# Kernel optimization log

Measured on AMD Instinct MI355X. Metric: run time of the kernel, lower is better.

Reference implementation:

```python
import jax, jax.numpy as jnp
from jax import lax
import numpy as np

# kz = (7, 3): kh is a 1x7 horizontal kernel, kv is a 3x1 vertical kernel
KH = (1, 7)
KV = (3, 1)


def _morph(x, ksz, op, init):
    # F.unfold zero-pads, so padded border values participate in the min/max
    ph, pw = ksz[0] // 2, ksz[1] // 2
    xp = jnp.pad(x, ((0, 0), (0, 0), (ph, ph), (pw, pw)))
    return lax.reduce_window(xp, init, op, (1, 1, ksz[0], ksz[1]), (1, 1, 1, 1), 'VALID')


def _erode(x, ksz):
    return _morph(x, ksz, lax.min, np.float32(np.inf))


def _dilate(x, ksz):
    return _morph(x, ksz, lax.max, np.float32(-np.inf))


def _calphi(x):
    dil = _dilate(x, KH)                                   # horizontal dilation (1x7)
    thr = dil.mean(axis=(2, 3), keepdims=True)             # per-image mean of dilation
    bi = ((x > thr) & (x == dil)).astype(x.dtype)          # horizontal local-max binarization
    return _dilate(_erode(bi, KV), KV)                     # morphological opening with 3x1


def setup_inputs() -> dict:
    key = jax.random.key(0)
    x = jax.random.normal(key, (8, 1, 2048, 2048), dtype=jnp.float32)
    return {"x": x}


def reference(x):
    s1 = _calphi(x).sum()
    s2 = _calphi(jnp.swapaxes(x, 2, 3)).sum()
    return s1 < s2
```

## Files before the change

### kernel.cpp

```cpp
#include <hip/hip_runtime.h>
#include <cstdint>

#define NEG_INF (-__builtin_inff())

static constexpr int H = 2048;
static constexpr int W = 2048;
static constexpr int STR = 248;
static constexpr int RC  = 8;
static constexpr int NR  = RC + 6;

struct F4 { float x, y, z, w; };

__device__ __forceinline__ F4 ld4(const float* __restrict__ p) {
    float4 v = *reinterpret_cast<const float4*>(p);
    return {v.x, v.y, v.z, v.w};
}

__device__ __forceinline__ float fmax3(float a, float b, float c) {
    return fmaxf(fmaxf(a, b), c);
}

__device__ __forceinline__ void hmax7_4(float a0, float a1, float a2,
                                        float a3, float a4, float a5, float a6,
                                        float a7, float a8, float a9,
                                        float& m0, float& m1, float& m2, float& m3) {
    float p23 = fmaxf(a2, a3), p45 = fmaxf(a4, a5), p67 = fmaxf(a6, a7);
    float q25 = fmaxf(p23, p45), q47 = fmaxf(p45, p67);
    m0 = fmax3(fmaxf(a0, a1), q25, a6);
    m1 = fmax3(fmaxf(a1, a2), fmax3(a3, a4, a5), fmaxf(a6, a7));
    m2 = fmax3(p23, q47, a8);
    m3 = fmax3(fmaxf(a3, a4), fmax3(a5, a6, a7), fmaxf(a8, a9));
}

struct Setup {
    int c4, cA, cmask, imask;
    float pad0, pad1, pad2, pad3;
};

__device__ __forceinline__ Setup make_setup(int sIdx, int lane) {
    Setup s;
    const int cstart = sIdx * STR;
    s.c4 = cstart - 4 + lane * 4;
    s.cA = min(max(s.c4, 0), W - 4);
    s.cmask = 0; s.imask = 0;
#pragma unroll
    for (int k = 0; k < 4; ++k) {
        const int col = s.c4 + k;
        if (col >= cstart && col < cstart + STR && col < W) s.cmask |= 1 << k;
        if (col >= 0 && col < W)                            s.imask |= 1 << k;
    }
    s.pad0 = ((s.c4 + 0) < 3 || (s.c4 + 0) > W - 4) ? 0.f : NEG_INF;
    s.pad1 = ((s.c4 + 1) < 3 || (s.c4 + 1) > W - 4) ? 0.f : NEG_INF;
    s.pad2 = ((s.c4 + 2) < 3 || (s.c4 + 2) > W - 4) ? 0.f : NEG_INF;
    s.pad3 = ((s.c4 + 3) < 3 || (s.c4 + 3) > W - 4) ? 0.f : NEG_INF;
    return s;
}

__device__ __forceinline__ void load_rows(const float* __restrict__ img,
                                          int r0, const Setup& s, F4 (&cur)[NR]) {
#pragma unroll
    for (int t = 0; t < NR; ++t) {
        const int irc = min(max(r0 - 3 + t, 0), H - 1);
        cur[t] = ld4(img + (size_t)irc * W + s.cA);
    }
#pragma unroll
    for (int t = 0; t < NR; ++t)
        asm volatile("" : "+v"(cur[t].x), "+v"(cur[t].y), "+v"(cur[t].z), "+v"(cur[t].w));
    if (s.imask != 0xF) {
#pragma unroll
        for (int t = 0; t < NR; ++t) {
            if (!(s.imask & 1)) cur[t].x = NEG_INF;
            if (!(s.imask & 2)) cur[t].y = NEG_INF;
            if (!(s.imask & 4)) cur[t].z = NEG_INF;
            if (!(s.imask & 8)) cur[t].w = NEG_INF;
        }
    }
#pragma unroll
    for (int t = 0; t < NR; ++t) {
        if (t < 3 || t >= NR - 3) {
            const int ir = r0 - 3 + t;
            if (ir < 0 || ir >= H) cur[t] = {NEG_INF, NEG_INF, NEG_INF, NEG_INF};
        }
    }
}

__global__ __launch_bounds__(256) void k_sums(const float* __restrict__ x,
                                              double* __restrict__ sums) {
    const int tid = threadIdx.x, lane = tid & 63, wid = tid >> 6;
    const int sIdx = blockIdx.x;
    const int rr   = blockIdx.y * 4 + wid;
    const int b    = blockIdx.z;
    const int r0   = rr * RC;
    const float* img = x + (size_t)b * H * W;
    const Setup s = make_setup(sIdx, lane);

    F4 cur[NR];
    load_rows(img, r0, s, cur);

    float shf = 0.f, svf = 0.f;
#pragma unroll
    for (int t = 3; t < 3 + RC; ++t) {
        F4 c = cur[t];
        float la1 = __shfl_up(c.y, 1), la2 = __shfl_up(c.z, 1), la3 = __shfl_up(c.w, 1);
        float ra0 = __shfl_down(c.x, 1), ra1 = __shfl_down(c.y, 1), ra2 = __shfl_down(c.z, 1);
        float m0, m1, m2, m3;
        hmax7_4(la1, la2, la3, c.x, c.y, c.z, c.w, ra0, ra1, ra2, m0, m1, m2, m3);
        m0 = fmaxf(m0, s.pad0); m1 = fmaxf(m1, s.pad1);
        m2 = fmaxf(m2, s.pad2); m3 = fmaxf(m3, s.pad3);
        shf += ((s.cmask & 1) ? m0 : 0.f) + ((s.cmask & 2) ? m1 : 0.f)
             + ((s.cmask & 4) ? m2 : 0.f) + ((s.cmask & 8) ? m3 : 0.f);
    }
#pragma unroll
    for (int jj = 0; jj < RC; ++jj) {
        const int j = r0 + jj;
        const float rpad = (j < 3 || j > H - 4) ? 0.f : NEG_INF;
        float mx = fmax3(fmax3(cur[jj].x, cur[jj+1].x, cur[jj+2].x),
                         fmax3(cur[jj+3].x, cur[jj+4].x, cur[jj+5].x), cur[jj+6].x);
        float my = fmax3(fmax3(cur[jj].y, cur[jj+1].y, cur[jj+2].y),
                         fmax3(cur[jj+3].y, cur[jj+4].y, cur[jj+5].y), cur[jj+6].y);
        float mz = fmax3(fmax3(cur[jj].z, cur[jj+1].z, cur[jj+2].z),
                         fmax3(cur[jj+3].z, cur[jj+4].z, cur[jj+5].z), cur[jj+6].z);
        float mw = fmax3(fmax3(cur[jj].w, cur[jj+1].w, cur[jj+2].w),
                         fmax3(cur[jj+3].w, cur[jj+4].w, cur[jj+5].w), cur[jj+6].w);
        mx = fmaxf(mx, rpad); my = fmaxf(my, rpad);
        mz = fmaxf(mz, rpad); mw = fmaxf(mw, rpad);
        svf += ((s.cmask & 1) ? mx : 0.f) + ((s.cmask & 2) ? my : 0.f)
             + ((s.cmask & 4) ? mz : 0.f) + ((s.cmask & 8) ? mw : 0.f);
    }

    double sh = (double)shf, sv = (double)svf;
    for (int off = 32; off > 0; off >>= 1) {
        sh += __shfl_down(sh, off);
        sv += __shfl_down(sv, off);
    }
    if (lane == 0) {
        const int bk = rr & 63;
        atomicAdd(&sums[(b)      * 64 + bk], sh);
        atomicAdd(&sums[(8 + b)  * 64 + bk], sv);
    }
}

__global__ void k_thr(const double* __restrict__ sums, float* __restrict__ thr) {
    const int p = threadIdx.x;
    if (p < 16) {
        const double* s = sums + p * 64;
        double a = 0.0;
        for (int i = 0; i < 64; ++i) a += s[i];
        thr[p] = (float)(a * (1.0 / ((double)H * (double)W)));
    }
}

__global__ __launch_bounds__(256) void k_counts(const float* __restrict__ x,
                                                const float* __restrict__ thr,
                                                unsigned int* __restrict__ cnts) {
    const int tid = threadIdx.x, lane = tid & 63, wid = tid >> 6;
    const int sIdx = blockIdx.x;
    const int rr   = blockIdx.y * 4 + wid;
    const int b    = blockIdx.z;
    const int r0   = rr * RC;
    const float* img = x + (size_t)b * H * W;
    const Setup s = make_setup(sIdx, lane);
    const float thr1 = thr[b], thr2 = thr[8 + b];

    F4 cur[NR];
    load_rows(img, r0, s, cur);

    unsigned bc0 = 0, bc1 = 0, bc2 = 0, bc3 = 0;
#pragma unroll
    for (int t = 1; t < NR - 1; ++t) {
        F4 c = cur[t];
        float la1 = __shfl_up(c.y, 1), la2 = __shfl_up(c.z, 1), la3 = __shfl_up(c.w, 1);
        float ra0 = __shfl_down(c.x, 1), ra1 = __shfl_down(c.y, 1), ra2 = __shfl_down(c.z, 1);
        float m0, m1, m2, m3;
        hmax7_4(la1, la2, la3, c.x, c.y, c.z, c.w, ra0, ra1, ra2, m0, m1, m2, m3);
        m0 = fmaxf(m0, s.pad0); m1 = fmaxf(m1, s.pad1);
        m2 = fmaxf(m2, s.pad2); m3 = fmaxf(m3, s.pad3);
        bc0 |= (c.x > thr1 && c.x == m0) ? (1u << t) : 0u;
        bc1 |= (c.y > thr1 && c.y == m1) ? (1u << t) : 0u;
        bc2 |= (c.z > thr1 && c.z == m2) ? (1u << t) : 0u;
        bc3 |= (c.w > thr1 && c.w == m3) ? (1u << t) : 0u;
    }
    const unsigned rowm = ((1u << RC) - 1u) << 3;
    unsigned e0 = bc0 & (bc0 << 1) & (bc0 >> 1);
    unsigned e1 = bc1 & (bc1 << 1) & (bc1 >> 1);
    unsigned e2 = bc2 & (bc2 << 1) & (bc2 >> 1);
    unsigned e3 = bc3 & (bc3 << 1) & (bc3 >> 1);
    unsigned o0 = e0 | (e0 << 1) | (e0 >> 1);
    unsigned o1_ = e1 | (e1 << 1) | (e1 >> 1);
    unsigned o2_ = e2 | (e2 << 1) | (e2 >> 1);
    unsigned o3_ = e3 | (e3 << 1) | (e3 >> 1);
    unsigned cnt1 = ((s.cmask & 1) ? __popc(o0  & rowm) : 0u)
                  + ((s.cmask & 2) ? __popc(o1_ & rowm) : 0u)
                  + ((s.cmask & 4) ? __popc(o2_ & rowm) : 0u)
                  + ((s.cmask & 8) ? __popc(o3_ & rowm) : 0u);

    unsigned d0 = 0, d1 = 0, d2 = 0, d3 = 0;
#pragma unroll
    for (int jj = 0; jj < RC; ++jj) {
        const int j = r0 + jj;
        const float rpad = (j < 3 || j > H - 4) ? 0.f : NEG_INF;
        float mx = fmax3(fmax3(cur[jj].x, cur[jj+1].x, cur[jj+2].x),
                         fmax3(cur[jj+3].x, cur[jj+4].x, cur[jj+5].x), cur[jj+6].x);
        float my = fmax3(fmax3(cur[jj].y, cur[jj+1].y, cur[jj+2].y),
                         fmax3(cur[jj+3].y, cur[jj+4].y, cur[jj+5].y), cur[jj+6].y);
        float mz = fmax3(fmax3(cur[jj].z, cur[jj+1].z, cur[jj+2].z),
                         fmax3(cur[jj+3].z, cur[jj+4].z, cur[jj+5].z), cur[jj+6].z);
        float mw = fmax3(fmax3(cur[jj].w, cur[jj+1].w, cur[jj+2].w),
                         fmax3(cur[jj+3].w, cur[jj+4].w, cur[jj+5].w), cur[jj+6].w);
        mx = fmaxf(mx, rpad); my = fmaxf(my, rpad);
        mz = fmaxf(mz, rpad); mw = fmaxf(mw, rpad);
        F4 ce = cur[jj + 3];
        d0 |= (ce.x > thr2 && ce.x == mx) ? (1u << jj) : 0u;
        d1 |= (ce.y > thr2 && ce.y == my) ? (1u << jj) : 0u;
        d2 |= (ce.z > thr2 && ce.z == mz) ? (1u << jj) : 0u;
        d3 |= (ce.w > thr2 && ce.w == mw) ? (1u << jj) : 0u;
    }
    const unsigned pz = __shfl_up(d2, 1), pw = __shfl_up(d3, 1);
    const unsigned n0 = __shfl_down(d0, 1), n1 = __shfl_down(d1, 1);
    const unsigned em1 = pz & pw & d0;
    const unsigned f0  = pw & d0 & d1;
    const unsigned f1  = d0 & d1 & d2;
    const unsigned f2  = d1 & d2 & d3;
    const unsigned f3  = d2 & d3 & n0;
    const unsigned fp4 = d3 & n0 & n1;
    const unsigned q0 = em1 | f0 | f1;
    const unsigned q1 = f0 | f1 | f2;
    const unsigned q2 = f1 | f2 | f3;
    const unsigned q3 = f2 | f3 | fp4;
    unsigned cnt2 = ((s.cmask & 1) ? __popc(q0) : 0u)
                  + ((s.cmask & 2) ? __popc(q1) : 0u)
                  + ((s.cmask & 4) ? __popc(q2) : 0u)
                  + ((s.cmask & 8) ? __popc(q3) : 0u);

    for (int off = 32; off > 0; off >>= 1) {
        cnt1 += __shfl_down(cnt1, off);
        cnt2 += __shfl_down(cnt2, off);
    }
    if (lane == 0) {
        const int bkt = (rr * 9 + sIdx) & 127;
        atomicAdd(&cnts[bkt],       cnt1);
        atomicAdd(&cnts[128 + bkt], cnt2);
    }
}

__global__ void k_final(const unsigned int* __restrict__ cnts,
                        int* __restrict__ out) {
    const int l = threadIdx.x;
    unsigned a = cnts[l] + cnts[64 + l];
    unsigned c = cnts[128 + l] + cnts[192 + l];
    for (int off = 32; off > 0; off >>= 1) {
        a += __shfl_down(a, off);
        c += __shfl_down(c, off);
    }
    if (l == 0) out[0] = (a < c) ? 1 : 0;
}

extern "C" void kernel_launch(void* const* d_in, const int* in_sizes, int n_in,
                              void* d_out, int out_size, void* d_ws, size_t ws_size,
                              hipStream_t stream) {
    const float* x = (const float*)d_in[0];
    int* out = (int*)d_out;
    double* sums = (double*)d_ws;
    float* thr = (float*)((char*)d_ws + 8192);
    unsigned int* cnts = (unsigned int*)((char*)d_ws + 8448);

    hipMemsetAsync(d_ws, 0, 16384, stream);

    k_sums  <<<dim3(9, 64, 8), 256, 0, stream>>>(x, sums);
    k_thr   <<<1, 16, 0, stream>>>(sums, thr);
    k_counts<<<dim3(9, 64, 8), 256, 0, stream>>>(x, thr, cnts);
    k_final <<<1, 64, 0, stream>>>(cnts, out);
}
```

Measured before the change: 247.1 us.

## Double rows per wave and replace atomics with per-block partial sums

Raises rows per wave from 8 to 16, which halves the grid and cuts the share of redundant halo-row loads (6 extra rows per chunk). Each block now reduces its four waves' results in shared memory and writes one slot per block, replacing global atomics into buckets and removing the workspace memset. The threshold and final kernels are rewritten to reduce over the per-block slots. The trade-offs are more registers per thread (22 float4 rows held) and fewer blocks to fill the GPU.

```diff
diff --git a/kernel.cpp b/kernel.cpp
--- a/kernel.cpp
+++ b/kernel.cpp
@@ -6,8 +6,11 @@
 static constexpr int H = 2048;
 static constexpr int W = 2048;
 static constexpr int STR = 248;
-static constexpr int RC  = 8;
+static constexpr int RC  = 16;
 static constexpr int NR  = RC + 6;
+static constexpr int NCH = H / RC;
+static constexpr int GY  = NCH / 4;
+static constexpr int NBLK = 9 * GY * 8;
 
 struct F4 { float x, y, z, w; };
 
@@ -82,6 +85,10 @@
             if (ir < 0 || ir >= H) cur[t] = {NEG_INF, NEG_INF, NEG_INF, NEG_INF};
         }
     }
+}
+
+__device__ __forceinline__ int blk_id() {
+    return (blockIdx.z * GY + blockIdx.y) * 9 + blockIdx.x;
 }
 
 __global__ __launch_bounds__(256) void k_sums(const float* __restrict__ x,
@@ -133,21 +140,28 @@
         sh += __shfl_down(sh, off);
         sv += __shfl_down(sv, off);
     }
-    if (lane == 0) {
-        const int bk = rr & 63;
-        atomicAdd(&sums[(b)      * 64 + bk], sh);
-        atomicAdd(&sums[(8 + b)  * 64 + bk], sv);
+    __shared__ double sdh[4], sdv[4];
+    if (lane == 0) { sdh[wid] = sh; sdv[wid] = sv; }
+    __syncthreads();
+    if (tid == 0) {
+        const int blk = blk_id();
+        sums[blk]        = sdh[0] + sdh[1] + sdh[2] + sdh[3];
+        sums[NBLK + blk] = sdv[0] + sdv[1] + sdv[2] + sdv[3];
     }
 }
 
 __global__ void k_thr(const double* __restrict__ sums, float* __restrict__ thr) {
-    const int p = threadIdx.x;
-    if (p < 16) {
-        const double* s = sums + p * 64;
-        double a = 0.0;
-        for (int i = 0; i < 64; ++i) a += s[i];
-        thr[p] = (float)(a * (1.0 / ((double)H * (double)W)));
-    }
+    const int tid = threadIdx.x;
+    const int pair = tid >> 4, l16 = tid & 15;
+    const double* base = sums + (pair < 8 ? pair * 288 : NBLK + (pair - 8) * 288);
+    double a = 0.0;
+#pragma unroll
+    for (int k = 0; k < 18; ++k) a += base[l16 + k * 16];
+    a += __shfl_down(a, 8);
+    a += __shfl_down(a, 4);
+    a += __shfl_down(a, 2);
+    a += __shfl_down(a, 1);
+    if (l16 == 0) thr[pair] = (float)(a * (1.0 / ((double)H * (double)W)));
 }
 
 __global__ __launch_bounds__(256) void k_counts(const float* __restrict__ x,
@@ -236,23 +250,37 @@
         cnt1 += __shfl_down(cnt1, off);
         cnt2 += __shfl_down(cnt2, off);
     }
-    if (lane == 0) {
-        const int bkt = (rr * 9 + sIdx) & 127;
-        atomicAdd(&cnts[bkt],       cnt1);
-        atomicAdd(&cnts[128 + bkt], cnt2);
+    __shared__ unsigned sc1[4], sc2[4];
+    if (lane == 0) { sc1[wid] = cnt1; sc2[wid] = cnt2; }
+    __syncthreads();
+    if (tid == 0) {
+        const int blk = blk_id();
+        cnts[blk]        = sc1[0] + sc1[1] + sc1[2] + sc1[3];
+        cnts[NBLK + blk] = sc2[0] + sc2[1] + sc2[2] + sc2[3];
     }
 }
 
 __global__ void k_final(const unsigned int* __restrict__ cnts,
                         int* __restrict__ out) {
-    const int l = threadIdx.x;
-    unsigned a = cnts[l] + cnts[64 + l];
-    unsigned c = cnts[128 + l] + cnts[192 + l];
+    const int tid = threadIdx.x;
+    unsigned a = 0, c = 0;
+    for (int i = tid; i < NBLK; i += 256) {
+        a += cnts[i];
+        c += cnts[NBLK + i];
+    }
     for (int off = 32; off > 0; off >>= 1) {
         a += __shfl_down(a, off);
         c += __shfl_down(c, off);
     }
-    if (l == 0) out[0] = (a < c) ? 1 : 0;
+    __shared__ unsigned sa[4], sc[4];
+    const int lane = tid & 63, wid = tid >> 6;
+    if (lane == 0) { sa[wid] = a; sc[wid] = c; }
+    __syncthreads();
+    if (tid == 0) {
+        unsigned A = sa[0] + sa[1] + sa[2] + sa[3];
+        unsigned C = sc[0] + sc[1] + sc[2] + sc[3];
+        out[0] = (A < C) ? 1 : 0;
+    }
 }
 
 extern "C" void kernel_launch(void* const* d_in, const int* in_sizes, int n_in,
@@ -261,13 +289,11 @@
     const float* x = (const float*)d_in[0];
     int* out = (int*)d_out;
     double* sums = (double*)d_ws;
-    float* thr = (float*)((char*)d_ws + 8192);
-    unsigned int* cnts = (unsigned int*)((char*)d_ws + 8448);
-
-    hipMemsetAsync(d_ws, 0, 16384, stream);
-
-    k_sums  <<<dim3(9, 64, 8), 256, 0, stream>>>(x, sums);
-    k_thr   <<<1, 16, 0, stream>>>(sums, thr);
-    k_counts<<<dim3(9, 64, 8), 256, 0, stream>>>(x, thr, cnts);
-    k_final <<<1, 64, 0, stream>>>(cnts, out);
-}
+    float* thr = (float*)((char*)d_ws + 2 * NBLK * 8);
+    unsigned int* cnts = (unsigned int*)((char*)d_ws + 2 * NBLK * 8 + 256);
+
+    k_sums  <<<dim3(9, GY, 8), 256, 0, stream>>>(x, sums);
+    k_thr   <<<1, 256, 0, stream>>>(sums, thr);
+    k_counts<<<dim3(9, GY, 8), 256, 0, stream>>>(x, thr, cnts);
+    k_final <<<1, 256, 0, stream>>>(cnts, out);
+}
```

New measurement: 265.3 us. 1.07x slower.

## Fuse four kernels into one cooperative persistent kernel with grid syncs

Applied to the files above, without the earlier changes.

Replaces the separate sums, threshold, counts and final kernels with one cooperative persistent kernel. Blocks loop over tasks and use grid-wide syncs between phases, and each block computes the thresholds itself into shared memory. This removes three kernel launch gaps and the tiny serial threshold and final kernels. The cost is two grid barriers and __launch_bounds__(256,4) register pressure, which may limit occupancy.

```diff
diff --git a/kernel.cpp b/kernel.cpp
--- a/kernel.cpp
+++ b/kernel.cpp
@@ -1,5 +1,8 @@
 #include <hip/hip_runtime.h>
+#include <hip/hip_cooperative_groups.h>
 #include <cstdint>
+
+namespace cg = cooperative_groups;
 
 #define NEG_INF (-__builtin_inff())
 
@@ -8,6 +11,8 @@
 static constexpr int STR = 248;
 static constexpr int RC  = 8;
 static constexpr int NR  = RC + 6;
+static constexpr int NCH = H / RC;
+static constexpr int NTASK = 9 * (NCH / 4) * 8;
 
 struct F4 { float x, y, z, w; };
 
@@ -84,175 +89,188 @@
     }
 }
 
-__global__ __launch_bounds__(256) void k_sums(const float* __restrict__ x,
-                                              double* __restrict__ sums) {
+__device__ __forceinline__ void task_decode(int beta, int& b, int& rrG, int& sIdx) {
+    b = beta / 576;
+    const int rem = beta % 576;
+    rrG = rem / 9;
+    sIdx = rem % 9;
+}
+
+__global__ __launch_bounds__(256, 4)
+void k_fused(const float* __restrict__ x, double* __restrict__ sums,
+             unsigned int* __restrict__ cnts, int* __restrict__ out) {
+    cg::grid_group grid = cg::this_grid();
     const int tid = threadIdx.x, lane = tid & 63, wid = tid >> 6;
-    const int sIdx = blockIdx.x;
-    const int rr   = blockIdx.y * 4 + wid;
-    const int b    = blockIdx.z;
-    const int r0   = rr * RC;
-    const float* img = x + (size_t)b * H * W;
-    const Setup s = make_setup(sIdx, lane);
-
-    F4 cur[NR];
-    load_rows(img, r0, s, cur);
-
-    float shf = 0.f, svf = 0.f;
-#pragma unroll
-    for (int t = 3; t < 3 + RC; ++t) {
-        F4 c = cur[t];
-        float la1 = __shfl_up(c.y, 1), la2 = __shfl_up(c.z, 1), la3 = __shfl_up(c.w, 1);
-        float ra0 = __shfl_down(c.x, 1), ra1 = __shfl_down(c.y, 1), ra2 = __shfl_down(c.z, 1);
-        float m0, m1, m2, m3;
-        hmax7_4(la1, la2, la3, c.x, c.y, c.z, c.w, ra0, ra1, ra2, m0, m1, m2, m3);
-        m0 = fmaxf(m0, s.pad0); m1 = fmaxf(m1, s.pad1);
-        m2 = fmaxf(m2, s.pad2); m3 = fmaxf(m3, s.pad3);
-        shf += ((s.cmask & 1) ? m0 : 0.f) + ((s.cmask & 2) ? m1 : 0.f)
-             + ((s.cmask & 4) ? m2 : 0.f) + ((s.cmask & 8) ? m3 : 0.f);
-    }
-#pragma unroll
-    for (int jj = 0; jj < RC; ++jj) {
-        const int j = r0 + jj;
-        const float rpad = (j < 3 || j > H - 4) ? 0.f : NEG_INF;
-        float mx = fmax3(fmax3(cur[jj].x, cur[jj+1].x, cur[jj+2].x),
-                         fmax3(cur[jj+3].x, cur[jj+4].x, cur[jj+5].x), cur[jj+6].x);
-        float my = fmax3(fmax3(cur[jj].y, cur[jj+1].y, cur[jj+2].y),
-                         fmax3(cur[jj+3].y, cur[jj+4].y, cur[jj+5].y), cur[jj+6].y);
-        float mz = fmax3(fmax3(cur[jj].z, cur[jj+1].z, cur[jj+2].z),
-                         fmax3(cur[jj+3].z, cur[jj+4].z, cur[jj+5].z), cur[jj+6].z);
-        float mw = fmax3(fmax3(cur[jj].w, cur[jj+1].w, cur[jj+2].w),
-                         fmax3(cur[jj+3].w, cur[jj+4].w, cur[jj+5].w), cur[jj+6].w);
-        mx = fmaxf(mx, rpad); my = fmaxf(my, rpad);
-        mz = fmaxf(mz, rpad); mw = fmaxf(mw, rpad);
-        svf += ((s.cmask & 1) ? mx : 0.f) + ((s.cmask & 2) ? my : 0.f)
-             + ((s.cmask & 4) ? mz : 0.f) + ((s.cmask & 8) ? mw : 0.f);
-    }
-
-    double sh = (double)shf, sv = (double)svf;
-    for (int off = 32; off > 0; off >>= 1) {
-        sh += __shfl_down(sh, off);
-        sv += __shfl_down(sv, off);
-    }
-    if (lane == 0) {
-        const int bk = rr & 63;
-        atomicAdd(&sums[(b)      * 64 + bk], sh);
-        atomicAdd(&sums[(8 + b)  * 64 + bk], sv);
-    }
-}
-
-__global__ void k_thr(const double* __restrict__ sums, float* __restrict__ thr) {
-    const int p = threadIdx.x;
-    if (p < 16) {
-        const double* s = sums + p * 64;
-        double a = 0.0;
-        for (int i = 0; i < 64; ++i) a += s[i];
-        thr[p] = (float)(a * (1.0 / ((double)H * (double)W)));
-    }
-}
-
-__global__ __launch_bounds__(256) void k_counts(const float* __restrict__ x,
-                                                const float* __restrict__ thr,
-                                                unsigned int* __restrict__ cnts) {
-    const int tid = threadIdx.x, lane = tid & 63, wid = tid >> 6;
-    const int sIdx = blockIdx.x;
-    const int rr   = blockIdx.y * 4 + wid;
-    const int b    = blockIdx.z;
-    const int r0   = rr * RC;
-    const float* img = x + (size_t)b * H * W;
-    const Setup s = make_setup(sIdx, lane);
-    const float thr1 = thr[b], thr2 = thr[8 + b];
-
-    F4 cur[NR];
-    load_rows(img, r0, s, cur);
-
-    unsigned bc0 = 0, bc1 = 0, bc2 = 0, bc3 = 0;
-#pragma unroll
-    for (int t = 1; t < NR - 1; ++t) {
-        F4 c = cur[t];
-        float la1 = __shfl_up(c.y, 1), la2 = __shfl_up(c.z, 1), la3 = __shfl_up(c.w, 1);
-        float ra0 = __shfl_down(c.x, 1), ra1 = __shfl_down(c.y, 1), ra2 = __shfl_down(c.z, 1);
-        float m0, m1, m2, m3;
-        hmax7_4(la1, la2, la3, c.x, c.y, c.z, c.w, ra0, ra1, ra2, m0, m1, m2, m3);
-        m0 = fmaxf(m0, s.pad0); m1 = fmaxf(m1, s.pad1);
-        m2 = fmaxf(m2, s.pad2); m3 = fmaxf(m3, s.pad3);
-        bc0 |= (c.x > thr1 && c.x == m0) ? (1u << t) : 0u;
-        bc1 |= (c.y > thr1 && c.y == m1) ? (1u << t) : 0u;
-        bc2 |= (c.z > thr1 && c.z == m2) ? (1u << t) : 0u;
-        bc3 |= (c.w > thr1 && c.w == m3) ? (1u << t) : 0u;
-    }
-    const unsigned rowm = ((1u << RC) - 1u) << 3;
-    unsigned e0 = bc0 & (bc0 << 1) & (bc0 >> 1);
-    unsigned e1 = bc1 & (bc1 << 1) & (bc1 >> 1);
-    unsigned e2 = bc2 & (bc2 << 1) & (bc2 >> 1);
-    unsigned e3 = bc3 & (bc3 << 1) & (bc3 >> 1);
-    unsigned o0 = e0 | (e0 << 1) | (e0 >> 1);
-    unsigned o1_ = e1 | (e1 << 1) | (e1 >> 1);
-    unsigned o2_ = e2 | (e2 << 1) | (e2 >> 1);
-    unsigned o3_ = e3 | (e3 << 1) | (e3 >> 1);
-    unsigned cnt1 = ((s.cmask & 1) ? __popc(o0  & rowm) : 0u)
-                  + ((s.cmask & 2) ? __popc(o1_ & rowm) : 0u)
-                  + ((s.cmask & 4) ? __popc(o2_ & rowm) : 0u)
-                  + ((s.cmask & 8) ? __popc(o3_ & rowm) : 0u);
-
-    unsigned d0 = 0, d1 = 0, d2 = 0, d3 = 0;
-#pragma unroll
-    for (int jj = 0; jj < RC; ++jj) {
-        const int j = r0 + jj;
-        const float rpad = (j < 3 || j > H - 4) ? 0.f : NEG_INF;
-        float mx = fmax3(fmax3(cur[jj].x, cur[jj+1].x, cur[jj+2].x),
-                         fmax3(cur[jj+3].x, cur[jj+4].x, cur[jj+5].x), cur[jj+6].x);
-        float my = fmax3(fmax3(cur[jj].y, cur[jj+1].y, cur[jj+2].y),
-                         fmax3(cur[jj+3].y, cur[jj+4].y, cur[jj+5].y), cur[jj+6].y);
-        float mz = fmax3(fmax3(cur[jj].z, cur[jj+1].z, cur[jj+2].z),
-                         fmax3(cur[jj+3].z, cur[jj+4].z, cur[jj+5].z), cur[jj+6].z);
-        float mw = fmax3(fmax3(cur[jj].w, cur[jj+1].w, cur[jj+2].w),
-                         fmax3(cur[jj+3].w, cur[jj+4].w, cur[jj+5].w), cur[jj+6].w);
-        mx = fmaxf(mx, rpad); my = fmaxf(my, rpad);
-        mz = fmaxf(mz, rpad); mw = fmaxf(mw, rpad);
-        F4 ce = cur[jj + 3];
-        d0 |= (ce.x > thr2 && ce.x == mx) ? (1u << jj) : 0u;
-        d1 |= (ce.y > thr2 && ce.y == my) ? (1u << jj) : 0u;
-        d2 |= (ce.z > thr2 && ce.z == mz) ? (1u << jj) : 0u;
-        d3 |= (ce.w > thr2 && ce.w == mw) ? (1u << jj) : 0u;
-    }
-    const unsigned pz = __shfl_up(d2, 1), pw = __shfl_up(d3, 1);
-    const unsigned n0 = __shfl_down(d0, 1), n1 = __shfl_down(d1, 1);
-    const unsigned em1 = pz & pw & d0;
-    const unsigned f0  = pw & d0 & d1;
-    const unsigned f1  = d0 & d1 & d2;
-    const unsigned f2  = d1 & d2 & d3;
-    const unsigned f3  = d2 & d3 & n0;
-    const unsigned fp4 = d3 & n0 & n1;
-    const unsigned q0 = em1 | f0 | f1;
-    const unsigned q1 = f0 | f1 | f2;
-    const unsigned q2 = f1 | f2 | f3;
-    const unsigned q3 = f2 | f3 | fp4;
-    unsigned cnt2 = ((s.cmask & 1) ? __popc(q0) : 0u)
-                  + ((s.cmask & 2) ? __popc(q1) : 0u)
-                  + ((s.cmask & 4) ? __popc(q2) : 0u)
-                  + ((s.cmask & 8) ? __popc(q3) : 0u);
-
-    for (int off = 32; off > 0; off >>= 1) {
-        cnt1 += __shfl_down(cnt1, off);
-        cnt2 += __shfl_down(cnt2, off);
-    }
-    if (lane == 0) {
-        const int bkt = (rr * 9 + sIdx) & 127;
-        atomicAdd(&cnts[bkt],       cnt1);
-        atomicAdd(&cnts[128 + bkt], cnt2);
-    }
-}
-
-__global__ void k_final(const unsigned int* __restrict__ cnts,
-                        int* __restrict__ out) {
-    const int l = threadIdx.x;
-    unsigned a = cnts[l] + cnts[64 + l];
-    unsigned c = cnts[128 + l] + cnts[192 + l];
-    for (int off = 32; off > 0; off >>= 1) {
-        a += __shfl_down(a, off);
-        c += __shfl_down(c, off);
-    }
-    if (l == 0) out[0] = (a < c) ? 1 : 0;
+    __shared__ float thrS[16];
+
+    for (int beta = blockIdx.x; beta < NTASK; beta += gridDim.x) {
+        int b, rrG, sIdx;
+        task_decode(beta, b, rrG, sIdx);
+        const int rr = rrG * 4 + wid, r0 = rr * RC;
+        const float* img = x + (size_t)b * H * W;
+        const Setup s = make_setup(sIdx, lane);
+
+        F4 cur[NR];
+        load_rows(img, r0, s, cur);
+
+        float shf = 0.f, svf = 0.f;
+#pragma unroll
+        for (int t = 3; t < 3 + RC; ++t) {
+            F4 c = cur[t];
+            float la1 = __shfl_up(c.y, 1), la2 = __shfl_up(c.z, 1), la3 = __shfl_up(c.w, 1);
+            float ra0 = __shfl_down(c.x, 1), ra1 = __shfl_down(c.y, 1), ra2 = __shfl_down(c.z, 1);
+            float m0, m1, m2, m3;
+            hmax7_4(la1, la2, la3, c.x, c.y, c.z, c.w, ra0, ra1, ra2, m0, m1, m2, m3);
+            m0 = fmaxf(m0, s.pad0); m1 = fmaxf(m1, s.pad1);
+            m2 = fmaxf(m2, s.pad2); m3 = fmaxf(m3, s.pad3);
+            shf += ((s.cmask & 1) ? m0 : 0.f) + ((s.cmask & 2) ? m1 : 0.f)
+                 + ((s.cmask & 4) ? m2 : 0.f) + ((s.cmask & 8) ? m3 : 0.f);
+        }
+#pragma unroll
+        for (int jj = 0; jj < RC; ++jj) {
+            const int j = r0 + jj;
+            const float rpad = (j < 3 || j > H - 4) ? 0.f : NEG_INF;
+            float mx = fmax3(fmax3(cur[jj].x, cur[jj+1].x, cur[jj+2].x),
+                             fmax3(cur[jj+3].x, cur[jj+4].x, cur[jj+5].x), cur[jj+6].x);
+            float my = fmax3(fmax3(cur[jj].y, cur[jj+1].y, cur[jj+2].y),
+                             fmax3(cur[jj+3].y, cur[jj+4].y, cur[jj+5].y), cur[jj+6].y);
+            float mz = fmax3(fmax3(cur[jj].z, cur[jj+1].z, cur[jj+2].z),
+                             fmax3(cur[jj+3].z, cur[jj+4].z, cur[jj+5].z), cur[jj+6].z);
+            float mw = fmax3(fmax3(cur[jj].w, cur[jj+1].w, cur[jj+2].w),
+                             fmax3(cur[jj+3].w, cur[jj+4].w, cur[jj+5].w), cur[jj+6].w);
+            mx = fmaxf(mx, rpad); my = fmaxf(my, rpad);
+            mz = fmaxf(mz, rpad); mw = fmaxf(mw, rpad);
+            svf += ((s.cmask & 1) ? mx : 0.f) + ((s.cmask & 2) ? my : 0.f)
+                 + ((s.cmask & 4) ? mz : 0.f) + ((s.cmask & 8) ? mw : 0.f);
+        }
+
+        double sh = (double)shf, sv = (double)svf;
+        for (int off = 32; off > 0; off >>= 1) {
+            sh += __shfl_down(sh, off);
+            sv += __shfl_down(sv, off);
+        }
+        if (lane == 0) {
+            const int bkt = (rr * 9 + sIdx) & 63;
+            atomicAdd(&sums[(b)     * 64 + bkt], sh);
+            atomicAdd(&sums[(8 + b) * 64 + bkt], sv);
+        }
+    }
+
+    __threadfence();
+    grid.sync();
+
+    {
+        const int pair = tid >> 4, l16 = tid & 15;
+        double a = sums[pair * 64 + l16]      + sums[pair * 64 + l16 + 16]
+                 + sums[pair * 64 + l16 + 32] + sums[pair * 64 + l16 + 48];
+        a += __shfl_down(a, 8);
+        a += __shfl_down(a, 4);
+        a += __shfl_down(a, 2);
+        a += __shfl_down(a, 1);
+        if (l16 == 0) thrS[pair] = (float)(a * (1.0 / ((double)H * (double)W)));
+    }
+    __syncthreads();
+
+    for (int beta = blockIdx.x; beta < NTASK; beta += gridDim.x) {
+        int b, rrG, sIdx;
+        task_decode(beta, b, rrG, sIdx);
+        const int rr = rrG * 4 + wid, r0 = rr * RC;
+        const float* img = x + (size_t)b * H * W;
+        const Setup s = make_setup(sIdx, lane);
+        const float thr1 = thrS[b], thr2 = thrS[8 + b];
+
+        F4 cur[NR];
+        load_rows(img, r0, s, cur);
+
+        unsigned bc0 = 0, bc1 = 0, bc2 = 0, bc3 = 0;
+#pragma unroll
+        for (int t = 1; t < NR - 1; ++t) {
+            F4 c = cur[t];
+            float la1 = __shfl_up(c.y, 1), la2 = __shfl_up(c.z, 1), la3 = __shfl_up(c.w, 1);
+            float ra0 = __shfl_down(c.x, 1), ra1 = __shfl_down(c.y, 1), ra2 = __shfl_down(c.z, 1);
+            float m0, m1, m2, m3;
+            hmax7_4(la1, la2, la3, c.x, c.y, c.z, c.w, ra0, ra1, ra2, m0, m1, m2, m3);
+            m0 = fmaxf(m0, s.pad0); m1 = fmaxf(m1, s.pad1);
+            m2 = fmaxf(m2, s.pad2); m3 = fmaxf(m3, s.pad3);
+            bc0 |= (c.x > thr1 && c.x == m0) ? (1u << t) : 0u;
+            bc1 |= (c.y > thr1 && c.y == m1) ? (1u << t) : 0u;
+            bc2 |= (c.z > thr1 && c.z == m2) ? (1u << t) : 0u;
+            bc3 |= (c.w > thr1 && c.w == m3) ? (1u << t) : 0u;
+        }
+        const unsigned rowm = ((1u << RC) - 1u) << 3;
+        unsigned e0 = bc0 & (bc0 << 1) & (bc0 >> 1);
+        unsigned e1 = bc1 & (bc1 << 1) & (bc1 >> 1);
+        unsigned e2 = bc2 & (bc2 << 1) & (bc2 >> 1);
+        unsigned e3 = bc3 & (bc3 << 1) & (bc3 >> 1);
+        unsigned o0  = e0 | (e0 << 1) | (e0 >> 1);
+        unsigned o1_ = e1 | (e1 << 1) | (e1 >> 1);
+        unsigned o2_ = e2 | (e2 << 1) | (e2 >> 1);
+        unsigned o3_ = e3 | (e3 << 1) | (e3 >> 1);
+        unsigned cnt1 = ((s.cmask & 1) ? __popc(o0  & rowm) : 0u)
+                      + ((s.cmask & 2) ? __popc(o1_ & rowm) : 0u)
+                      + ((s.cmask & 4) ? __popc(o2_ & rowm) : 0u)
+                      + ((s.cmask & 8) ? __popc(o3_ & rowm) : 0u);
+
+        unsigned d0 = 0, d1 = 0, d2 = 0, d3 = 0;
+#pragma unroll
+        for (int jj = 0; jj < RC; ++jj) {
+            const int j = r0 + jj;
+            const float rpad = (j < 3 || j > H - 4) ? 0.f : NEG_INF;
+            float mx = fmax3(fmax3(cur[jj].x, cur[jj+1].x, cur[jj+2].x),
+                             fmax3(cur[jj+3].x, cur[jj+4].x, cur[jj+5].x), cur[jj+6].x);
+            float my = fmax3(fmax3(cur[jj].y, cur[jj+1].y, cur[jj+2].y),
+                             fmax3(cur[jj+3].y, cur[jj+4].y, cur[jj+5].y), cur[jj+6].y);
+            float mz = fmax3(fmax3(cur[jj].z, cur[jj+1].z, cur[jj+2].z),
+                             fmax3(cur[jj+3].z, cur[jj+4].z, cur[jj+5].z), cur[jj+6].z);
+            float mw = fmax3(fmax3(cur[jj].w, cur[jj+1].w, cur[jj+2].w),
+                             fmax3(cur[jj+3].w, cur[jj+4].w, cur[jj+5].w), cur[jj+6].w);
+            mx = fmaxf(mx, rpad); my = fmaxf(my, rpad);
+            mz = fmaxf(mz, rpad); mw = fmaxf(mw, rpad);
+            F4 ce = cur[jj + 3];
+            d0 |= (ce.x > thr2 && ce.x == mx) ? (1u << jj) : 0u;
+            d1 |= (ce.y > thr2 && ce.y == my) ? (1u << jj) : 0u;
+            d2 |= (ce.z > thr2 && ce.z == mz) ? (1u << jj) : 0u;
+            d3 |= (ce.w > thr2 && ce.w == mw) ? (1u << jj) : 0u;
+        }
+        const unsigned pz = __shfl_up(d2, 1), pw = __shfl_up(d3, 1);
+        const unsigned n0 = __shfl_down(d0, 1), n1 = __shfl_down(d1, 1);
+        const unsigned em1 = pz & pw & d0;
+        const unsigned f0  = pw & d0 & d1;
+        const unsigned f1  = d0 & d1 & d2;
+        const unsigned f2  = d1 & d2 & d3;
+        const unsigned f3  = d2 & d3 & n0;
+        const unsigned fp4 = d3 & n0 & n1;
+        const unsigned q0 = em1 | f0 | f1;
+        const unsigned q1 = f0 | f1 | f2;
+        const unsigned q2 = f1 | f2 | f3;
+        const unsigned q3 = f2 | f3 | fp4;
+        unsigned cnt2 = ((s.cmask & 1) ? __popc(q0) : 0u)
+                      + ((s.cmask & 2) ? __popc(q1) : 0u)
+                      + ((s.cmask & 4) ? __popc(q2) : 0u)
+                      + ((s.cmask & 8) ? __popc(q3) : 0u);
+
+        for (int off = 32; off > 0; off >>= 1) {
+            cnt1 += __shfl_down(cnt1, off);
+            cnt2 += __shfl_down(cnt2, off);
+        }
+        if (lane == 0) {
+            const int bkt = (rr * 9 + sIdx) & 63;
+            atomicAdd(&cnts[bkt],      cnt1);
+            atomicAdd(&cnts[64 + bkt], cnt2);
+        }
+    }
+
+    __threadfence();
+    grid.sync();
+
+    if (blockIdx.x == 0 && tid < 64) {
+        unsigned a = cnts[tid], c = cnts[64 + tid];
+        for (int off = 32; off > 0; off >>= 1) {
+            a += __shfl_down(a, off);
+            c += __shfl_down(c, off);
+        }
+        if (tid == 0) out[0] = (a < c) ? 1 : 0;
+    }
 }
 
 extern "C" void kernel_launch(void* const* d_in, const int* in_sizes, int n_in,
@@ -261,13 +279,18 @@
     const float* x = (const float*)d_in[0];
     int* out = (int*)d_out;
     double* sums = (double*)d_ws;
-    float* thr = (float*)((char*)d_ws + 8192);
-    unsigned int* cnts = (unsigned int*)((char*)d_ws + 8448);
-
-    hipMemsetAsync(d_ws, 0, 16384, stream);
-
-    k_sums  <<<dim3(9, 64, 8), 256, 0, stream>>>(x, sums);
-    k_thr   <<<1, 16, 0, stream>>>(sums, thr);
-    k_counts<<<dim3(9, 64, 8), 256, 0, stream>>>(x, thr, cnts);
-    k_final <<<1, 64, 0, stream>>>(cnts, out);
-}
+    unsigned int* cnts = (unsigned int*)((char*)d_ws + 8192);
+
+    hipMemsetAsync(d_ws, 0, 8192 + 512, stream);
+
+    int maxBlocksPerCU = 0;
+    hipOccupancyMaxActiveBlocksPerMultiprocessor(&maxBlocksPerCU,
+                                                 (const void*)k_fused, 256, 0);
+    if (maxBlocksPerCU <= 0) maxBlocksPerCU = 2;
+    int grid = maxBlocksPerCU * 256;
+    if (grid > NTASK) grid = NTASK;
+
+    void* args[] = {(void*)&x, (void*)&sums, (void*)&cnts, (void*)&out};
+    hipLaunchCooperativeKernel((const void*)k_fused, dim3(grid), dim3(256),
+                               args, 0, stream);
+}
```

After: 614.2 us. 2.49x slower.
